# Kernel optimization log

Measured on AMD Instinct MI355X. Metric: run time of the kernel, lower is better.

The kernel has to match this reference:

```python
import jax, jax.numpy as jnp
import numpy as np

N, E, F_IN, H0, H1 = 50000, 800000, 128, 128, 64


def setup_inputs() -> dict:
    key = jax.random.key(0)
    k1, k2, k3, k4, k5, k6 = jax.random.split(key, 6)
    node_features = jax.random.normal(k1, (N, F_IN), dtype=jnp.float32)
    edges = jax.random.randint(k2, (E, 2), 0, N, dtype=jnp.int64)
    # GCNConv params (glorot-ish scale)
    W1 = jax.random.normal(k3, (F_IN, H0), dtype=jnp.float32) / np.sqrt(F_IN)
    b1 = jnp.zeros((H0,), dtype=jnp.float32)
    W2 = jax.random.normal(k4, (H0, H1), dtype=jnp.float32) / np.sqrt(H0)
    b2 = jnp.zeros((H1,), dtype=jnp.float32)
    return {"node_features": node_features, "edges": edges,
            "W1": W1, "b1": b1, "W2": W2, "b2": b2}


def reference(node_features, edges, W1, b1, W2, b2):
    # GCNConv: out = D^{-1/2} (A + I) D^{-1/2} (X W) + b, with self-loops.
    n = node_features.shape[0]
    ei = edges.T  # [2, E] like edge_index.t() in the torch code
    self_idx = jnp.arange(n, dtype=ei.dtype)
    src = jnp.concatenate([ei[0], self_idx])  # [E+N]
    dst = jnp.concatenate([ei[1], self_idx])  # [E+N]
    deg = jnp.zeros((n,), node_features.dtype).at[dst].add(1.0)  # >=1 (self-loops)
    dinv = jax.lax.rsqrt(deg)
    norm = (dinv[src] * dinv[dst])[:, None]  # [E+N, 1]

    def gcn(x, W, b):
        h = x @ W                      # dense transform [n, d_out]
        msg = h[src] * norm            # gather + scale  [E+N, d_out]
        agg = jax.ops.segment_sum(msg, dst, num_segments=n)  # scatter-add
        return agg + b

    x = jax.nn.relu(gcn(node_features, W1, b1))
    # F.dropout(training=self.training): identity in eval mode (deterministic ref)
    x = gcn(x, W2, b2)
    return x
```

## Files before the change

kernel.cpp:

```cpp
#include <hip/hip_runtime.h>
#include <hip/hip_bf16.h>


#define NCHUNK 128

#define OFF_ROWSTART (size_t)0x0
#define OFF_DINV     (size_t)0x40000
#define OFF_BLOCKSUM (size_t)0x80000
#define OFF_FLAG     (size_t)0x80800
#define OFF_LRANK    (size_t)0x81000
#define OFF_CSR      (size_t)0x150000
#define OFF_H        (size_t)0x300000
#define OFF_W1T      (size_t)0xA00000
#define OFF_W2T      (size_t)0xA10000
#define OFF_BUFA     (size_t)0xB00000
#define OFF_BUFB     (size_t)0x1800000

typedef short bf16x8 __attribute__((ext_vector_type(8)));
typedef float f32x4 __attribute__((ext_vector_type(4)));

__device__ __forceinline__ float2 bf2f(unsigned u) {
    float2 r;
    r.x = __uint_as_float(u << 16);
    r.y = __uint_as_float(u & 0xffff0000u);
    return r;
}
__device__ __forceinline__ unsigned f2bf(float a, float b) {
    __hip_bfloat162 h = __float22bfloat162_rn(make_float2(a, b));
    union { __hip_bfloat162 h; unsigned u; } cv;
    cv.h = h;
    return cv.u;
}

__global__ void k_convW(const float* __restrict__ W1, const float* __restrict__ W2,
                        unsigned short* __restrict__ W1T,
                        unsigned short* __restrict__ W2T) {
    const int t = threadIdx.x, b = blockIdx.x;
    const int k0 = (t & 15) * 8;
    if (b < 8) {
        int nn = b * 16 + (t >> 4);
        float w[8];
#pragma unroll
        for (int j = 0; j < 8; ++j) w[j] = W1[(size_t)(k0 + j) * 128 + nn];
        uint4 q;
        q.x = f2bf(w[0], w[1]); q.y = f2bf(w[2], w[3]);
        q.z = f2bf(w[4], w[5]); q.w = f2bf(w[6], w[7]);
        *reinterpret_cast<uint4*>(&W1T[(size_t)nn * 128 + k0]) = q;
    } else {
        int nn = (b - 8) * 16 + (t >> 4);
        float w[8];
#pragma unroll
        for (int j = 0; j < 8; ++j) w[j] = W2[(size_t)(k0 + j) * 64 + nn];
        uint4 q;
        q.x = f2bf(w[0], w[1]); q.y = f2bf(w[2], w[3]);
        q.z = f2bf(w[4], w[5]); q.w = f2bf(w[6], w[7]);
        *reinterpret_cast<uint4*>(&W2T[(size_t)nn * 128 + k0]) = q;
    }
}

__global__ __launch_bounds__(256) void k_hist(const int* __restrict__ e32, int E,
                                              int chunk, int n,
                                              unsigned char* __restrict__ lrank,
                                              unsigned char* __restrict__ H,
                                              int* __restrict__ flag) {
    __shared__ unsigned h[12544];
    __shared__ int anyv;
    const int t = threadIdx.x, b = blockIdx.x;
    const int nw = (n + 3) >> 2;
    if (t == 0) anyv = 0;
    for (int i = t; i < nw; i += 256) h[i] = 0u;
    __syncthreads();
    const int e0 = b * chunk, e1 = min(E, e0 + chunk);
    int v = 0;
    const int lim = min(e1, e0 + 2048);
    for (int e = e0 + t; e < lim; e += 256) v |= e32[2 * e + 1];
    if (v) atomicOr(&anyv, 1);
    __syncthreads();
    const int f = (anyv == 0) ? 1 : 0;
    if (b == 0 && t == 0) *flag = f;
    for (int e = e0 + t; e < e1; e += 256) {
        int dst;
        if (f) dst = reinterpret_cast<const int4*>(e32)[e].z;
        else   dst = reinterpret_cast<const int2*>(e32)[e].y;
        int sh = (dst & 3) << 3;
        unsigned old = atomicAdd(&h[dst >> 2], 1u << sh);
        lrank[e] = (unsigned char)((old >> sh) & 0xffu);
    }
    __syncthreads();
    unsigned* Hp = reinterpret_cast<unsigned*>(H);
    const size_t wbase = (size_t)b * (size_t)(n >> 2);
    for (int i = t; i < (n >> 2); i += 256) Hp[wbase + i] = h[i];
}

__global__ __launch_bounds__(256) void k_mergescan(
        unsigned char* __restrict__ H, int n,
        float* __restrict__ dinv, int* __restrict__ rowstart,
        int* __restrict__ blocksum) {
    __shared__ int sh[256];
    const int t = threadIdx.x;
    const int bin0 = blockIdx.x * 1024 + 4 * t;
    int s0 = 0, s1 = 0, s2 = 0, s3 = 0;
    if (bin0 < n) {
        unsigned* Hp = reinterpret_cast<unsigned*>(H);
        const size_t wstride = (size_t)(n >> 2);
        const size_t widx = (size_t)(bin0 >> 2);
#pragma unroll 8
        for (int b = 0; b < NCHUNK; ++b) {
            size_t idx = (size_t)b * wstride + widx;
            unsigned w = Hp[idx];
            Hp[idx] = (unsigned)s0 | ((unsigned)s1 << 8) |
                      ((unsigned)s2 << 16) | ((unsigned)s3 << 24);
            s0 += (int)(w & 0xffu);
            s1 += (int)((w >> 8) & 0xffu);
            s2 += (int)((w >> 16) & 0xffu);
            s3 += (int)((w >> 24) & 0xffu);
        }
        float4 dv;
        dv.x = rsqrtf((float)s0 + 1.0f);
        dv.y = rsqrtf((float)s1 + 1.0f);
        dv.z = rsqrtf((float)s2 + 1.0f);
        dv.w = rsqrtf((float)s3 + 1.0f);
        *reinterpret_cast<float4*>(dinv + bin0) = dv;
    }
    int tot = s0 + s1 + s2 + s3;
    sh[t] = tot;
    __syncthreads();
    for (int off = 1; off < 256; off <<= 1) {
        int add = (t >= off) ? sh[t - off] : 0;
        __syncthreads();
        sh[t] += add;
        __syncthreads();
    }
    if (bin0 < n) {
        int ex = sh[t] - tot;
        int4 rs;
        rs.x = ex;
        rs.y = ex + s0;
        rs.z = ex + s0 + s1;
        rs.w = ex + s0 + s1 + s2;
        *reinterpret_cast<int4*>(rowstart + bin0) = rs;
    }
    if (t == 255) blocksum[blockIdx.x] = sh[255];
}

__global__ void k_scan2(int* __restrict__ blocksum, int nb) {
    __shared__ int sh[256];
    int t = threadIdx.x;
    int v = (t < nb) ? blocksum[t] : 0;
    sh[t] = v;
    __syncthreads();
    for (int off = 1; off < 256; off <<= 1) {
        int add = (t >= off) ? sh[t - off] : 0;
        __syncthreads();
        sh[t] += add;
        __syncthreads();
    }
    if (t < nb) blocksum[t] = sh[t] - v;
}

__global__ void k_scan3(int* __restrict__ rowstart, int n,
                        const int* __restrict__ blocksum, int E) {
    int i = blockIdx.x * 256 + threadIdx.x;
    if (i < n) rowstart[i] += blocksum[i >> 10];
    if (i == 0) rowstart[n] = E;
}

__global__ void k_fill(const int* __restrict__ e32, int E, int chunk,
                       const int* __restrict__ flag,
                       const int* __restrict__ rowstart,
                       const unsigned char* __restrict__ H, int n,
                       const unsigned char* __restrict__ lrank,
                       unsigned short* __restrict__ csr) {
    int e = blockIdx.x * 256 + threadIdx.x;
    if (e >= E) return;
    int b = blockIdx.x / (chunk >> 8);
    int f = *flag;
    int src, dst;
    if (f) { int4 v = reinterpret_cast<const int4*>(e32)[e]; src = v.x; dst = v.z; }
    else   { int2 v = reinterpret_cast<const int2*>(e32)[e]; src = v.x; dst = v.y; }
    csr[rowstart[dst] + (int)H[(size_t)b * n + dst] + (int)lrank[e]] =
        (unsigned short)src;
}

__global__ __launch_bounds__(256) void k_gemm1m(const float* __restrict__ X,
                                                const unsigned short* __restrict__ W1T,
                                                const float* __restrict__ dinv,
                                                unsigned short* __restrict__ out,
                                                int n) {
    __shared__ unsigned short Xs[64 * 136];
    __shared__ unsigned short Ws[128 * 136];
    const int t = threadIdx.x;
    const int row0 = blockIdx.x * 64;
#pragma unroll
    for (int it = 0; it < 8; ++it) {
        int i = t + it * 256;
        int r = i >> 4, c8 = i & 15;
        *reinterpret_cast<uint4*>(&Ws[r * 136 + c8 * 8]) =
            *reinterpret_cast<const uint4*>(&W1T[(size_t)r * 128 + c8 * 8]);
    }
#pragma unroll
    for (int it = 0; it < 8; ++it) {
        int i = t + it * 256;
        int r = i >> 5, c4 = i & 31;
        int gr = row0 + r;
        float4 v = make_float4(0.f, 0.f, 0.f, 0.f);
        if (gr < n) v = *reinterpret_cast<const float4*>(&X[(size_t)gr * 128 + c4 * 4]);
        uint2 q;
        q.x = f2bf(v.x, v.y);
        q.y = f2bf(v.z, v.w);
        *reinterpret_cast<uint2*>(&Xs[r * 136 + c4 * 4]) = q;
    }
    __syncthreads();
    const int w = t >> 6, lane = t & 63;
    const int m = lane & 15, kg = lane >> 4;
    f32x4 acc[8] = {};
#pragma unroll
    for (int kt = 0; kt < 128; kt += 32) {
        bf16x8 a = *reinterpret_cast<const bf16x8*>(&Xs[(w * 16 + m) * 136 + kt + kg * 8]);
#pragma unroll
        for (int j = 0; j < 8; ++j) {
            bf16x8 bb = *reinterpret_cast<const bf16x8*>(&Ws[(j * 16 + m) * 136 + kt + kg * 8]);
            acc[j] = __builtin_amdgcn_mfma_f32_16x16x32_bf16(a, bb, acc[j], 0, 0, 0);
        }
    }
    const int rbase = row0 + w * 16 + kg * 4;
#pragma unroll
    for (int r = 0; r < 4; ++r) {
        int gr = rbase + r;
        if (gr < n) {
            float dv = dinv[gr];
#pragma unroll
            for (int j = 0; j < 8; ++j)
                out[(size_t)gr * 128 + j * 16 + m] =
                    (unsigned short)(f2bf(acc[j][r] * dv, 0.f) & 0xffffu);
        }
    }
}

__global__ __launch_bounds__(256) void k_gemm2m(const unsigned short* __restrict__ X1,
                                                const unsigned short* __restrict__ W2T,
                                                const float* __restrict__ dinv,
                                                unsigned short* __restrict__ out,
                                                int n) {
    __shared__ unsigned short Xs[64 * 136];
    __shared__ unsigned short Ws[64 * 136];
    const int t = threadIdx.x;
    const int row0 = blockIdx.x * 64;
#pragma unroll
    for (int it = 0; it < 4; ++it) {
        int i = t + it * 256;
        int r = i >> 4, c8 = i & 15;
        *reinterpret_cast<uint4*>(&Ws[r * 136 + c8 * 8]) =
            *reinterpret_cast<const uint4*>(&W2T[(size_t)r * 128 + c8 * 8]);
    }
#pragma unroll
    for (int it = 0; it < 4; ++it) {
        int i = t + it * 256;
        int r = i >> 4, c8 = i & 15;
        int gr = row0 + r;
        uint4 q = make_uint4(0u, 0u, 0u, 0u);
        if (gr < n) q = *reinterpret_cast<const uint4*>(&X1[(size_t)gr * 128 + c8 * 8]);
        *reinterpret_cast<uint4*>(&Xs[r * 136 + c8 * 8]) = q;
    }
    __syncthreads();
    const int w = t >> 6, lane = t & 63;
    const int m = lane & 15, kg = lane >> 4;
    f32x4 acc[4] = {};
#pragma unroll
    for (int kt = 0; kt < 128; kt += 32) {
        bf16x8 a = *reinterpret_cast<const bf16x8*>(&Xs[(w * 16 + m) * 136 + kt + kg * 8]);
#pragma unroll
        for (int j = 0; j < 4; ++j) {
            bf16x8 bb = *reinterpret_cast<const bf16x8*>(&Ws[(j * 16 + m) * 136 + kt + kg * 8]);
            acc[j] = __builtin_amdgcn_mfma_f32_16x16x32_bf16(a, bb, acc[j], 0, 0, 0);
        }
    }
    const int rbase = row0 + w * 16 + kg * 4;
#pragma unroll
    for (int r = 0; r < 4; ++r) {
        int gr = rbase + r;
        if (gr < n) {
            float dv = dinv[gr];
#pragma unroll
            for (int j = 0; j < 4; ++j)
                out[(size_t)gr * 64 + j * 16 + m] =
                    (unsigned short)(f2bf(acc[j][r] * dv, 0.f) & 0xffffu);
        }
    }
}

__global__ __launch_bounds__(256) void k_spmm128(
        const unsigned* __restrict__ H32, const int* __restrict__ rowstart,
        const unsigned short* __restrict__ csr, const float* __restrict__ dinv,
        const float* __restrict__ bias, unsigned* __restrict__ out, int n) {
    int node = blockIdx.x * 4 + (threadIdx.x >> 6);
    if (node >= n) return;
    int lane = threadIdx.x & 63;
    float di = dinv[node];
    float2 acc = bf2f(H32[(size_t)node * 64 + lane]);
    int s0 = rowstart[node], s1 = rowstart[node + 1];
    for (int j = s0; j < s1; j += 8) {
        int srcs[8];
        unsigned uu[8];
#pragma unroll
        for (int u = 0; u < 8; ++u) srcs[u] = csr[min(j + u, s1 - 1)];
#pragma unroll
        for (int u = 0; u < 8; ++u) uu[u] = H32[(size_t)srcs[u] * 64 + lane];
#pragma unroll
        for (int u = 0; u < 8; ++u) {
            float2 fv = bf2f(uu[u]);
            bool ok = (j + u) < s1;
            acc.x += ok ? fv.x : 0.f;
            acc.y += ok ? fv.y : 0.f;
        }
    }
    float2 b = reinterpret_cast<const float2*>(bias)[lane];
    float ox = fmaxf(fmaf(di, acc.x, b.x), 0.f);
    float oy = fmaxf(fmaf(di, acc.y, b.y), 0.f);
    out[(size_t)node * 64 + lane] = f2bf(ox, oy);
}

__global__ __launch_bounds__(256) void k_spmm64(
        const unsigned* __restrict__ H32, const int* __restrict__ rowstart,
        const unsigned short* __restrict__ csr, const float* __restrict__ dinv,
        const float* __restrict__ bias, float* __restrict__ out, int n) {
    int node = blockIdx.x * 8 + (threadIdx.x >> 5);
    if (node >= n) return;
    int f2 = threadIdx.x & 31;
    float di = dinv[node];
    float2 acc = bf2f(H32[(size_t)node * 32 + f2]);
    int s0 = rowstart[node], s1 = rowstart[node + 1];
    for (int j = s0; j < s1; j += 8) {
        int srcs[8];
        unsigned uu[8];
#pragma unroll
        for (int u = 0; u < 8; ++u) srcs[u] = csr[min(j + u, s1 - 1)];
#pragma unroll
        for (int u = 0; u < 8; ++u) uu[u] = H32[(size_t)srcs[u] * 32 + f2];
#pragma unroll
        for (int u = 0; u < 8; ++u) {
            float2 fv = bf2f(uu[u]);
            bool ok = (j + u) < s1;
            acc.x += ok ? fv.x : 0.f;
            acc.y += ok ? fv.y : 0.f;
        }
    }
    float2 b = reinterpret_cast<const float2*>(bias)[f2];
    float2 o;
    o.x = fmaf(di, acc.x, b.x);
    o.y = fmaf(di, acc.y, b.y);
    reinterpret_cast<float2*>(out)[(size_t)node * 32 + f2] = o;
}

extern "C" void kernel_launch(void* const* d_in, const int* in_sizes, int n_in,
                              void* d_out, int out_size, void* d_ws, size_t ws_size,
                              hipStream_t stream) {
    const float* X   = (const float*)d_in[0];
    const int*   e32 = (const int*)d_in[1];
    const float* W1  = (const float*)d_in[2];
    const float* b1  = (const float*)d_in[3];
    const float* W2  = (const float*)d_in[4];
    const float* b2  = (const float*)d_in[5];
    float* out = (float*)d_out;

    const int n = in_sizes[0] / 128;
    const int E = in_sizes[1] / 2;
    const int chunk = (((E + NCHUNK - 1) / NCHUNK) + 255) & ~255;

    char* ws = (char*)d_ws;
    int*            rowstart = (int*)(ws + OFF_ROWSTART);
    float*          dinv     = (float*)(ws + OFF_DINV);
    int*            blocksum = (int*)(ws + OFF_BLOCKSUM);
    int*            flag     = (int*)(ws + OFF_FLAG);
    unsigned char*  lrank    = (unsigned char*)(ws + OFF_LRANK);
    unsigned short* csr      = (unsigned short*)(ws + OFF_CSR);
    unsigned char*  H        = (unsigned char*)(ws + OFF_H);
    unsigned short* W1T      = (unsigned short*)(ws + OFF_W1T);
    unsigned short* W2T      = (unsigned short*)(ws + OFF_W2T);
    unsigned short* bufA     = (unsigned short*)(ws + OFF_BUFA);
    unsigned*       bufB     = (unsigned*)(ws + OFF_BUFB);

    const int NB   = (n + 255) / 256;
    const int NBms = (n + 1023) / 1024;
    const int EB   = (E + 255) / 256;
    const int RB   = (n + 63) / 64;

    k_convW<<<12, 256, 0, stream>>>(W1, W2, W1T, W2T);
    k_hist<<<NCHUNK, 256, 0, stream>>>(e32, E, chunk, n, lrank, H, flag);
    k_mergescan<<<NBms, 256, 0, stream>>>(H, n, dinv, rowstart, blocksum);
    k_scan2<<<1, 256, 0, stream>>>(blocksum, NBms);
    k_scan3<<<NB, 256, 0, stream>>>(rowstart, n, blocksum, E);
    k_fill<<<EB, 256, 0, stream>>>(e32, E, chunk, flag, rowstart, H, n, lrank, csr);

    k_gemm1m<<<RB, 256, 0, stream>>>(X, W1T, dinv, bufA, n);
    k_spmm128<<<(n + 3) / 4, 256, 0, stream>>>((const unsigned*)bufA, rowstart, csr,
                                               dinv, b1, bufB, n);
    k_gemm2m<<<RB, 256, 0, stream>>>((const unsigned short*)bufB, W2T, dinv, bufA, n);
    k_spmm64<<<(n + 7) / 8, 256, 0, stream>>>((const unsigned*)bufA, rowstart, csr,
                                              dinv, b2, out, n);
}
```

Baseline: 137.3 us.

## Fold weight conversion into histogram, merge scan kernels, widen SpMM gathers

Weight transpose/convert blocks are appended to the histogram launch, and the single-block blocksum scan is folded into the rowstart add kernel, where each block redundantly scans the blocksums serially. This removes two kernel launches. Both SpMM kernels now have each thread gather 4 bf16 features (8 bytes) instead of 2, which halves the threads per node and doubles the nodes per block. The aim is fewer launches and wider memory transactions, at the cost of less parallelism per row and redundant serial scan work in every block.

```diff
diff --git a/kernel.cpp b/kernel.cpp
--- a/kernel.cpp
+++ b/kernel.cpp
@@ -32,40 +32,42 @@
     return cv.u;
 }
 
-__global__ void k_convW(const float* __restrict__ W1, const float* __restrict__ W2,
-                        unsigned short* __restrict__ W1T,
-                        unsigned short* __restrict__ W2T) {
-    const int t = threadIdx.x, b = blockIdx.x;
-    const int k0 = (t & 15) * 8;
-    if (b < 8) {
-        int nn = b * 16 + (t >> 4);
-        float w[8];
-#pragma unroll
-        for (int j = 0; j < 8; ++j) w[j] = W1[(size_t)(k0 + j) * 128 + nn];
-        uint4 q;
-        q.x = f2bf(w[0], w[1]); q.y = f2bf(w[2], w[3]);
-        q.z = f2bf(w[4], w[5]); q.w = f2bf(w[6], w[7]);
-        *reinterpret_cast<uint4*>(&W1T[(size_t)nn * 128 + k0]) = q;
-    } else {
-        int nn = (b - 8) * 16 + (t >> 4);
-        float w[8];
-#pragma unroll
-        for (int j = 0; j < 8; ++j) w[j] = W2[(size_t)(k0 + j) * 64 + nn];
-        uint4 q;
-        q.x = f2bf(w[0], w[1]); q.y = f2bf(w[2], w[3]);
-        q.z = f2bf(w[4], w[5]); q.w = f2bf(w[6], w[7]);
-        *reinterpret_cast<uint4*>(&W2T[(size_t)nn * 128 + k0]) = q;
-    }
-}
-
 __global__ __launch_bounds__(256) void k_hist(const int* __restrict__ e32, int E,
                                               int chunk, int n,
                                               unsigned char* __restrict__ lrank,
                                               unsigned char* __restrict__ H,
-                                              int* __restrict__ flag) {
+                                              int* __restrict__ flag,
+                                              const float* __restrict__ W1,
+                                              const float* __restrict__ W2,
+                                              unsigned short* __restrict__ W1T,
+                                              unsigned short* __restrict__ W2T) {
+    const int t = threadIdx.x, b = blockIdx.x;
+    if (b >= NCHUNK) {
+        const int bb = b - NCHUNK;
+        const int k0 = (t & 15) * 8;
+        if (bb < 8) {
+            int nn = bb * 16 + (t >> 4);
+            float w[8];
+#pragma unroll
+            for (int j = 0; j < 8; ++j) w[j] = W1[(size_t)(k0 + j) * 128 + nn];
+            uint4 q;
+            q.x = f2bf(w[0], w[1]); q.y = f2bf(w[2], w[3]);
+            q.z = f2bf(w[4], w[5]); q.w = f2bf(w[6], w[7]);
+            *reinterpret_cast<uint4*>(&W1T[(size_t)nn * 128 + k0]) = q;
+        } else {
+            int nn = (bb - 8) * 16 + (t >> 4);
+            float w[8];
+#pragma unroll
+            for (int j = 0; j < 8; ++j) w[j] = W2[(size_t)(k0 + j) * 64 + nn];
+            uint4 q;
+            q.x = f2bf(w[0], w[1]); q.y = f2bf(w[2], w[3]);
+            q.z = f2bf(w[4], w[5]); q.w = f2bf(w[6], w[7]);
+            *reinterpret_cast<uint4*>(&W2T[(size_t)nn * 128 + k0]) = q;
+        }
+        return;
+    }
     __shared__ unsigned h[12544];
     __shared__ int anyv;
-    const int t = threadIdx.x, b = blockIdx.x;
     const int nw = (n + 3) >> 2;
     if (t == 0) anyv = 0;
     for (int i = t; i < nw; i += 256) h[i] = 0u;
@@ -143,25 +145,20 @@
     if (t == 255) blocksum[blockIdx.x] = sh[255];
 }
 
-__global__ void k_scan2(int* __restrict__ blocksum, int nb) {
-    __shared__ int sh[256];
+__global__ void k_scan3(int* __restrict__ rowstart, int n,
+                        const int* __restrict__ blocksum, int nb, int E) {
+    __shared__ int bs[65];
     int t = threadIdx.x;
-    int v = (t < nb) ? blocksum[t] : 0;
-    sh[t] = v;
-    __syncthreads();
-    for (int off = 1; off < 256; off <<= 1) {
-        int add = (t >= off) ? sh[t - off] : 0;
-        __syncthreads();
-        sh[t] += add;
-        __syncthreads();
-    }
-    if (t < nb) blocksum[t] = sh[t] - v;
-}
-
-__global__ void k_scan3(int* __restrict__ rowstart, int n,
-                        const int* __restrict__ blocksum, int E) {
-    int i = blockIdx.x * 256 + threadIdx.x;
-    if (i < n) rowstart[i] += blocksum[i >> 10];
+    if (t < nb) bs[t + 1] = blocksum[t];
+    if (t == 0) bs[0] = 0;
+    __syncthreads();
+    if (t == 0) {
+        int s = 0;
+        for (int k = 1; k <= nb; ++k) { s += bs[k]; bs[k] = s; }
+    }
+    __syncthreads();
+    int i = blockIdx.x * 256 + t;
+    if (i < n) rowstart[i] += bs[i >> 10];
     if (i == 0) rowstart[n] = E;
 }
 
@@ -293,63 +290,80 @@
         const unsigned* __restrict__ H32, const int* __restrict__ rowstart,
         const unsigned short* __restrict__ csr, const float* __restrict__ dinv,
         const float* __restrict__ bias, unsigned* __restrict__ out, int n) {
-    int node = blockIdx.x * 4 + (threadIdx.x >> 6);
+    int node = blockIdx.x * 8 + (threadIdx.x >> 5);
     if (node >= n) return;
-    int lane = threadIdx.x & 63;
+    int f2 = threadIdx.x & 31;
+    const uint2* H2 = reinterpret_cast<const uint2*>(H32);
     float di = dinv[node];
-    float2 acc = bf2f(H32[(size_t)node * 64 + lane]);
+    uint2 sv = H2[(size_t)node * 32 + f2];
+    float2 a0 = bf2f(sv.x), a1 = bf2f(sv.y);
+    float acc0 = a0.x, acc1 = a0.y, acc2 = a1.x, acc3 = a1.y;
     int s0 = rowstart[node], s1 = rowstart[node + 1];
     for (int j = s0; j < s1; j += 8) {
         int srcs[8];
-        unsigned uu[8];
+        uint2 uu[8];
 #pragma unroll
         for (int u = 0; u < 8; ++u) srcs[u] = csr[min(j + u, s1 - 1)];
 #pragma unroll
-        for (int u = 0; u < 8; ++u) uu[u] = H32[(size_t)srcs[u] * 64 + lane];
+        for (int u = 0; u < 8; ++u) uu[u] = H2[(size_t)srcs[u] * 32 + f2];
 #pragma unroll
         for (int u = 0; u < 8; ++u) {
-            float2 fv = bf2f(uu[u]);
+            float2 f0 = bf2f(uu[u].x), f1 = bf2f(uu[u].y);
             bool ok = (j + u) < s1;
-            acc.x += ok ? fv.x : 0.f;
-            acc.y += ok ? fv.y : 0.f;
-        }
-    }
-    float2 b = reinterpret_cast<const float2*>(bias)[lane];
-    float ox = fmaxf(fmaf(di, acc.x, b.x), 0.f);
-    float oy = fmaxf(fmaf(di, acc.y, b.y), 0.f);
-    out[(size_t)node * 64 + lane] = f2bf(ox, oy);
+            acc0 += ok ? f0.x : 0.f;
+            acc1 += ok ? f0.y : 0.f;
+            acc2 += ok ? f1.x : 0.f;
+            acc3 += ok ? f1.y : 0.f;
+        }
+    }
+    float4 b = reinterpret_cast<const float4*>(bias)[f2];
+    float o0 = fmaxf(fmaf(di, acc0, b.x), 0.f);
+    float o1 = fmaxf(fmaf(di, acc1, b.y), 0.f);
+    float o2 = fmaxf(fmaf(di, acc2, b.z), 0.f);
+    float o3 = fmaxf(fmaf(di, acc3, b.w), 0.f);
+    uint2 q;
+    q.x = f2bf(o0, o1);
+    q.y = f2bf(o2, o3);
+    reinterpret_cast<uint2*>(out)[(size_t)node * 32 + f2] = q;
 }
 
 __global__ __launch_bounds__(256) void k_spmm64(
         const unsigned* __restrict__ H32, const int* __restrict__ rowstart,
         const unsigned short* __restrict__ csr, const float* __restrict__ dinv,
         const float* __restrict__ bias, float* __restrict__ out, int n) {
-    int node = blockIdx.x * 8 + (threadIdx.x >> 5);
+    int node = blockIdx.x * 16 + (threadIdx.x >> 4);
     if (node >= n) return;
-    int f2 = threadIdx.x & 31;
+    int f2 = threadIdx.x & 15;
+    const uint2* H2 = reinterpret_cast<const uint2*>(H32);
     float di = dinv[node];
-    float2 acc = bf2f(H32[(size_t)node * 32 + f2]);
+    uint2 sv = H2[(size_t)node * 16 + f2];
+    float2 a0 = bf2f(sv.x), a1 = bf2f(sv.y);
+    float acc0 = a0.x, acc1 = a0.y, acc2 = a1.x, acc3 = a1.y;
     int s0 = rowstart[node], s1 = rowstart[node + 1];
     for (int j = s0; j < s1; j += 8) {
         int srcs[8];
-        unsigned uu[8];
+        uint2 uu[8];
 #pragma unroll
         for (int u = 0; u < 8; ++u) srcs[u] = csr[min(j + u, s1 - 1)];
 #pragma unroll
-        for (int u = 0; u < 8; ++u) uu[u] = H32[(size_t)srcs[u] * 32 + f2];
+        for (int u = 0; u < 8; ++u) uu[u] = H2[(size_t)srcs[u] * 16 + f2];
 #pragma unroll
         for (int u = 0; u < 8; ++u) {
-            float2 fv = bf2f(uu[u]);
+            float2 f0 = bf2f(uu[u].x), f1 = bf2f(uu[u].y);
             bool ok = (j + u) < s1;
-            acc.x += ok ? fv.x : 0.f;
-            acc.y += ok ? fv.y : 0.f;
-        }
-    }
-    float2 b = reinterpret_cast<const float2*>(bias)[f2];
-    float2 o;
-    o.x = fmaf(di, acc.x, b.x);
-    o.y = fmaf(di, acc.y, b.y);
-    reinterpret_cast<float2*>(out)[(size_t)node * 32 + f2] = o;
+            acc0 += ok ? f0.x : 0.f;
+            acc1 += ok ? f0.y : 0.f;
+            acc2 += ok ? f1.x : 0.f;
+            acc3 += ok ? f1.y : 0.f;
+        }
+    }
+    float4 b = reinterpret_cast<const float4*>(bias)[f2];
+    float4 o;
+    o.x = fmaf(di, acc0, b.x);
+    o.y = fmaf(di, acc1, b.y);
+    o.z = fmaf(di, acc2, b.z);
+    o.w = fmaf(di, acc3, b.w);
+    reinterpret_cast<float4*>(out)[(size_t)node * 16 + f2] = o;
 }
 
 extern "C" void kernel_launch(void* const* d_in, const int* in_sizes, int n_in,
@@ -385,17 +399,16 @@
     const int EB   = (E + 255) / 256;
     const int RB   = (n + 63) / 64;
 
-    k_convW<<<12, 256, 0, stream>>>(W1, W2, W1T, W2T);
-    k_hist<<<NCHUNK, 256, 0, stream>>>(e32, E, chunk, n, lrank, H, flag);
+    k_hist<<<NCHUNK + 12, 256, 0, stream>>>(e32, E, chunk, n, lrank, H, flag,
+                                            W1, W2, W1T, W2T);
     k_mergescan<<<NBms, 256, 0, stream>>>(H, n, dinv, rowstart, blocksum);
-    k_scan2<<<1, 256, 0, stream>>>(blocksum, NBms);
-    k_scan3<<<NB, 256, 0, stream>>>(rowstart, n, blocksum, E);
+    k_scan3<<<NB, 256, 0, stream>>>(rowstart, n, blocksum, NBms, E);
     k_fill<<<EB, 256, 0, stream>>>(e32, E, chunk, flag, rowstart, H, n, lrank, csr);
 
     k_gemm1m<<<RB, 256, 0, stream>>>(X, W1T, dinv, bufA, n);
-    k_spmm128<<<(n + 3) / 4, 256, 0, stream>>>((const unsigned*)bufA, rowstart, csr,
+    k_spmm128<<<(n + 7) / 8, 256, 0, stream>>>((const unsigned*)bufA, rowstart, csr,
                                                dinv, b1, bufB, n);
     k_gemm2m<<<RB, 256, 0, stream>>>((const unsigned short*)bufB, W2T, dinv, bufA, n);
-    k_spmm64<<<(n + 7) / 8, 256, 0, stream>>>((const unsigned*)bufA, rowstart, csr,
-                                              dinv, b2, out, n);
-}
+    k_spmm64<<<(n + 15) / 16, 256, 0, stream>>>((const unsigned*)bufA, rowstart, csr,
+                                                dinv, b2, out, n);
+}
```

Result: faster. 127.8 us (-6.9%).
